# Kernel optimization log

Hardware: AMD Instinct MI355X
Metric: run time of the kernel (lower is better)

Reference implementation:

```python
import jax, jax.numpy as jnp
import numpy as np

EPS_NORM = 1e-12   # torch F.normalize eps
EPS_BN = 1e-5      # BatchNorm1d eps
NEG_SLOPE = 0.01   # LeakyReLU default


def _l2_normalize(x, axis):
    # torch F.normalize: x / max(||x||, eps)
    n = jnp.sqrt(jnp.sum(x * x, axis=axis, keepdims=True))
    return x / jnp.maximum(n, EPS_NORM)


def setup_inputs() -> dict:
    key = jax.random.key(0)
    k1, k2, k3, k4, k5, k6, k7 = jax.random.split(key, 7)
    B, C, N, M, OUT = 8, 128, 4096, 4096, 128
    return {
        "input": jax.random.normal(k1, (B, C, N), dtype=jnp.float32),
        "target_g": jax.random.normal(k2, (B, C, M), dtype=jnp.float32),
        "weight": jax.random.normal(k3, (C, OUT), dtype=jnp.float32) * (1.0 / np.sqrt(OUT)),
        "gamma": jax.random.normal(k4, (OUT,), dtype=jnp.float32),
        "beta": jax.random.normal(k5, (OUT,), dtype=jnp.float32),
        "running_mean": jax.random.normal(k6, (OUT,), dtype=jnp.float32),
        "running_var": jax.random.uniform(k7, (OUT,), dtype=jnp.float32, minval=0.5, maxval=1.5),
    }


def reference(input, target_g, weight, gamma, beta, running_mean, running_var):
    # input: [B, C, N], target_g: [B, C, M]
    # cosine-similarity adjacency: [B, M, N]
    tg = _l2_normalize(target_g, axis=1)
    inp_n = _l2_normalize(input, axis=1)
    adj = jnp.einsum('bcm,bcn->bmn', tg, inp_n)
    adj = jax.nn.softmax(adj, axis=-1)
    # aggregate: [B, M, C]
    agg = jnp.einsum('bmn,bcn->bmc', adj, input)
    # project: [B, M, OUT] -> permute to [B, OUT, M]
    out = jnp.einsum('bmc,co->bom', agg, weight)
    # LeakyReLU then BatchNorm1d (eval mode, running stats)
    out = jnp.where(out >= 0, out, NEG_SLOPE * out)
    inv = jax.lax.rsqrt(running_var + EPS_BN)
    out = (out - running_mean[None, :, None]) * (inv * gamma)[None, :, None] + beta[None, :, None]
    return out
```

## Files before the change

### kernel.cpp

```cpp
#include <hip/hip_runtime.h>
#include <hip/hip_bf16.h>

#define BATCH 8
#define CDIM 128
#define NDIM 4096

typedef __bf16 bf16x8 __attribute__((ext_vector_type(8)));
typedef float f32x4 __attribute__((ext_vector_type(4)));
typedef float f32x16 __attribute__((ext_vector_type(16)));
typedef unsigned u32x4 __attribute__((ext_vector_type(4)));

#define QT_OFF 0u
#define KT_OFF 8388608u
#define VB_OFF 16777216u
#define WT_OFF 25165824u
#define SC_OFF (WT_OFF + 32768u)
#define BI_OFF (SC_OFF + 512u)

__device__ __forceinline__ f32x4 mfma16(bf16x8 a, bf16x8 b, f32x4 c) {
    return __builtin_amdgcn_mfma_f32_16x16x32_bf16(a, b, c, 0, 0, 0);
}
__device__ __forceinline__ f32x16 mfma32(bf16x8 a, bf16x8 b, f32x16 c) {
    return __builtin_amdgcn_mfma_f32_32x32x16_bf16(a, b, c, 0, 0, 0);
}

__device__ __forceinline__ unsigned pack2bf(float a, float b) {
    unsigned short ul = __builtin_bit_cast(unsigned short, (__bf16)a);
    unsigned short uh = __builtin_bit_cast(unsigned short, (__bf16)b);
    return (unsigned)ul | ((unsigned)uh << 16);
}

__device__ __forceinline__ void glds16(const void* g, void* l) {
    __builtin_amdgcn_global_load_lds((__attribute__((address_space(1))) void*)(void*)g,
                                     (__attribute__((address_space(3))) void*)l, 16, 0, 0);
}

__global__ __launch_bounds__(256) void prep_nt(const float* __restrict__ input,
                                               const float* __restrict__ tg,
                                               const float* __restrict__ wgt,
                                               const float* __restrict__ gamma,
                                               const float* __restrict__ beta,
                                               const float* __restrict__ mean,
                                               const float* __restrict__ var,
                                               void* __restrict__ ws) {
    __shared__ float Tt[64][129];
    __shared__ float psum[4][64];
    __shared__ float rn[64];
    const int n0 = blockIdx.x * 64;
    const int b  = blockIdx.y;
    const int tid = threadIdx.x;
    const float* src = (blockIdx.z == 0 ? input : tg) + (size_t)b * CDIM * NDIM;

    #pragma unroll
    for (int i = 0; i < 8; ++i) {
        int f = tid + i * 256;
        int c = f >> 4, j4 = f & 15;
        float4 v = *(const float4*)(src + (size_t)c * NDIM + n0 + j4 * 4);
        Tt[j4 * 4 + 0][c] = v.x;
        Tt[j4 * 4 + 1][c] = v.y;
        Tt[j4 * 4 + 2][c] = v.z;
        Tt[j4 * 4 + 3][c] = v.w;
    }
    __syncthreads();
    {
        int j = tid & 63, part = tid >> 6;
        float ss = 0.f;
        #pragma unroll 8
        for (int c = part * 32; c < part * 32 + 32; ++c) { float x = Tt[j][c]; ss += x * x; }
        psum[part][j] = ss;
    }
    __syncthreads();
    if (tid < 64) {
        float s = psum[0][tid] + psum[1][tid] + psum[2][tid] + psum[3][tid];
        rn[tid] = 1.0f / fmaxf(sqrtf(s), 1e-12f);
    }
    __syncthreads();

    __hip_bfloat16* dstT = (__hip_bfloat16*)((char*)ws + (blockIdx.z == 0 ? KT_OFF : QT_OFF))
                           + ((size_t)b * NDIM + n0) * CDIM;
    #pragma unroll
    for (int i = 0; i < 8; ++i) {
        int f = tid + i * 256;
        int j = f >> 5, c4 = f & 31;
        float r = rn[j];
        float4 v = *(const float4*)&Tt[j][c4 * 4];
        uint2 pk; pk.x = pack2bf(v.x * r, v.y * r); pk.y = pack2bf(v.z * r, v.w * r);
        *(uint2*)((unsigned short*)dstT + (size_t)j * CDIM + c4 * 4) = pk;
    }
    if (blockIdx.z == 0) {
        __hip_bfloat16* vb = (__hip_bfloat16*)((char*)ws + VB_OFF) + (size_t)b * CDIM * NDIM + n0;
        #pragma unroll
        for (int i = 0; i < 8; ++i) {
            int f = tid + i * 256;
            int c = f >> 4, j4 = f & 15;
            float x0 = Tt[j4 * 4 + 0][c], x1 = Tt[j4 * 4 + 1][c];
            float x2 = Tt[j4 * 4 + 2][c], x3 = Tt[j4 * 4 + 3][c];
            uint2 pv; pv.x = pack2bf(x0, x1); pv.y = pack2bf(x2, x3);
            *(uint2*)((unsigned short*)vb + (size_t)c * NDIM + j4 * 4) = pv;
        }
    } else if (blockIdx.x == 0 && b == 0) {
        __hip_bfloat16* wT = (__hip_bfloat16*)((char*)ws + WT_OFF);
        float* sc = (float*)((char*)ws + SC_OFF);
        float* bi = (float*)((char*)ws + BI_OFF);
        #pragma unroll
        for (int i = 0; i < 64; ++i) {
            int f = tid + i * 256;
            int c = f >> 7, o = f & 127;
            wT[o * 128 + c] = __hip_bfloat16(wgt[c * 128 + o]);
        }
        if (tid < 128) {
            float inv = rsqrtf(var[tid] + 1e-5f);
            float s = inv * gamma[tid];
            sc[tid] = s;
            bi[tid] = beta[tid] - mean[tid] * s;
        }
    }
}

__global__ __launch_bounds__(512, 2) void flash5(const void* __restrict__ ws_,
                                                 float* __restrict__ out) {
    extern __shared__ char smem[];
    const char* ws = (const char*)ws_;
    const __hip_bfloat16* Qt = (const __hip_bfloat16*)(ws + QT_OFF);
    const __hip_bfloat16* Kt = (const __hip_bfloat16*)(ws + KT_OFF);
    const __hip_bfloat16* Vb = (const __hip_bfloat16*)(ws + VB_OFF);
    const __hip_bfloat16* wT = (const __hip_bfloat16*)(ws + WT_OFF);
    const float* scale = (const float*)(ws + SC_OFF);
    const float* bias  = (const float*)(ws + BI_OFF);

    const int bx = blockIdx.x;
    const int b  = bx & 7;
    const int m0 = (bx >> 3) * 128;
    const int tid = threadIdx.x;
    const int w = tid >> 6, lane = tid & 63;
    const int hf = lane >> 5;
    const int l31 = lane & 31;
    const int nt = w & 1;
    const int mt = w >> 1;

    const char* kgb = (const char*)(Kt + (size_t)b * NDIM * CDIM);
    const char* vgb = (const char*)(Vb + (size_t)b * CDIM * NDIM);

    bf16x8 qb[8];
    {
        const char* qrow = (const char*)Qt + ((size_t)b * NDIM + m0 + mt * 32 + l31) * 256 + hf * 16;
        #pragma unroll
        for (int s = 0; s < 8; ++s) qb[s] = *(const bf16x8*)(qrow + s * 32);
    }

    unsigned kOff[8];
    {
        int nn = nt * 32 + l31;
        #pragma unroll
        for (int s = 0; s < 8; ++s)
            kOff[s] = nn * 256 + (((2 * s + hf) ^ (nn & 15)) * 16);
    }
    unsigned vOff[2][4];
    #pragma unroll
    for (int t = 0; t < 2; ++t)
        #pragma unroll
        for (int ca = 0; ca < 4; ++ca) {
            int c = ca * 32 + l31;
            vOff[t][ca] = 16384 + c * 128 + (((nt * 4 + t * 2 + hf) ^ (c & 7)) * 16);
        }

    const char* kSrc[2]; const char* vSrc[2];
    unsigned kDst[2], vDst[2];
    #pragma unroll
    for (int i = 0; i < 2; ++i) {
        int slot = i * 512 + tid;
        int n = slot >> 4, j = slot & 15;
        kSrc[i] = kgb + n * 256 + ((j ^ (n & 15)) * 16);
        kDst[i] = i * 8192 + w * 1024;
        int c = slot >> 3, j8 = slot & 7;
        vSrc[i] = vgb + (size_t)c * 8192 + ((j8 ^ (c & 7)) * 16);
        vDst[i] = 16384 + i * 8192 + w * 1024;
    }

    f32x16 oacc[4];
    #pragma unroll
    for (int ca = 0; ca < 4; ++ca)
        #pragma unroll
        for (int i = 0; i < 16; ++i) oacc[ca][i] = 0.f;
    float lacc = 0.f;

    #pragma unroll
    for (int i = 0; i < 2; ++i) { glds16(kSrc[i], smem + kDst[i]); kSrc[i] += 16384; }
    #pragma unroll
    for (int i = 0; i < 2; ++i) { glds16(vSrc[i], smem + vDst[i]); vSrc[i] += 128; }

    auto body = [&](const unsigned bo, const bool do_pref) {
        asm volatile("s_waitcnt vmcnt(0) lgkmcnt(0)\ns_barrier" ::: "memory");
        if (do_pref) {
            const unsigned obo = bo ^ 32768u;
            #pragma unroll
            for (int i = 0; i < 2; ++i) { glds16(kSrc[i], smem + (obo + kDst[i])); kSrc[i] += 16384; }
            #pragma unroll
            for (int i = 0; i < 2; ++i) { glds16(vSrc[i], smem + (obo + vDst[i])); vSrc[i] += 128; }
        }

        f32x16 st;
        #pragma unroll
        for (int i = 0; i < 16; ++i) st[i] = 0.f;
        #pragma unroll
        for (int s = 0; s < 8; ++s) {
            bf16x8 kf = *(const bf16x8*)(smem + bo + kOff[s]);
            st = mfma32(kf, qb[s], st);
        }

        unsigned d[8];
        float lsum = 0.f;
        #pragma unroll
        for (int rq = 0; rq < 4; ++rq) {
            float e0 = __expf(st[rq * 4 + 0] - 1.0f);
            float e1 = __expf(st[rq * 4 + 1] - 1.0f);
            float e2 = __expf(st[rq * 4 + 2] - 1.0f);
            float e3 = __expf(st[rq * 4 + 3] - 1.0f);
            lsum += (e0 + e1) + (e2 + e3);
            d[rq * 2 + 0] = pack2bf(e0, e1);
            d[rq * 2 + 1] = pack2bf(e2, e3);
        }
        lacc += lsum;
        unsigned o[8];
        #pragma unroll
        for (int j = 0; j < 8; ++j) o[j] = (unsigned)__shfl_xor((int)d[j], 32, 64);
        bf16x8 pf[2];
        #pragma unroll
        for (int t = 0; t < 2; ++t) {
            u32x4 tv;
            tv.x = hf ? o[4 * t + 2] : d[4 * t + 0];
            tv.y = hf ? o[4 * t + 3] : d[4 * t + 1];
            tv.z = hf ? d[4 * t + 2] : o[4 * t + 0];
            tv.w = hf ? d[4 * t + 3] : o[4 * t + 1];
            pf[t] = __builtin_bit_cast(bf16x8, tv);
        }

        #pragma unroll
        for (int t = 0; t < 2; ++t) {
            #pragma unroll
            for (int ca = 0; ca < 4; ++ca) {
                bf16x8 vf = *(const bf16x8*)(smem + bo + vOff[t][ca]);
                oacc[ca] = mfma32(vf, pf[t], oacc[ca]);
            }
        }
    };

    for (int ii = 0; ii < 32; ++ii) {
        body(0u, true);
        body(32768u, ii != 31);
    }

    float lw = lacc + __shfl_xor(lacc, 32, 64);
    __syncthreads();
    float* lLds = (float*)(smem + 65536);
    if (lane < 32) lLds[w * 32 + lane] = lw;
    if (w & 1) {
        float4* dst = (float4*)smem + (w >> 1) * 1024 + lane;
        #pragma unroll
        for (int ca = 0; ca < 4; ++ca)
            #pragma unroll
            for (int rq = 0; rq < 4; ++rq) {
                float4 t = { oacc[ca][rq * 4 + 0], oacc[ca][rq * 4 + 1],
                             oacc[ca][rq * 4 + 2], oacc[ca][rq * 4 + 3] };
                dst[(ca * 4 + rq) * 64] = t;
            }
    }
    __syncthreads();
    char* sAgg = smem + 67584;
    if (!(w & 1)) {
        float linv = 1.0f / (lLds[w * 32 + l31] + lLds[(w + 1) * 32 + l31]);
        const float4* srcp = (const float4*)smem + (w >> 1) * 1024 + lane;
        int m = (w >> 1) * 32 + l31;
        char* aggRow = sAgg + m * 256;
        const int mx = (m & 7) << 1;
        #pragma unroll
        for (int ca = 0; ca < 4; ++ca)
            #pragma unroll
            for (int rq = 0; rq < 4; ++rq) {
                float4 ov = srcp[(ca * 4 + rq) * 64];
                float v0 = (oacc[ca][rq * 4 + 0] + ov.x) * linv;
                float v1 = (oacc[ca][rq * 4 + 1] + ov.y) * linv;
                float v2 = (oacc[ca][rq * 4 + 2] + ov.z) * linv;
                float v3 = (oacc[ca][rq * 4 + 3] + ov.w) * linv;
                int cq = ca * 8 + rq * 2 + hf;
                uint2 pk; pk.x = pack2bf(v0, v1); pk.y = pack2bf(v2, v3);
                *(uint2*)(aggRow + ((cq ^ mx) * 8)) = pk;
            }
    }
    __syncthreads();

    const int li = lane & 15, q = lane >> 4;
    const int pm = w * 16 + li;
    f32x4 racc[8];
    #pragma unroll
    for (int ob = 0; ob < 8; ++ob) { racc[ob][0]=0.f; racc[ob][1]=0.f; racc[ob][2]=0.f; racc[ob][3]=0.f; }
    #pragma unroll
    for (int ks = 0; ks < 4; ++ks) {
        int slot8 = ((ks * 4 + q) * 2) ^ ((li & 7) << 1);
        bf16x8 af = *(const bf16x8*)(sAgg + pm * 256 + slot8 * 8);
        #pragma unroll
        for (int ob = 0; ob < 8; ++ob) {
            bf16x8 wf = *(const bf16x8*)((const char*)wT + (ob * 16 + li) * 256 + ks * 64 + q * 16);
            racc[ob] = mfma16(af, wf, racc[ob]);
        }
    }

    float* sRes = (float*)smem;
    #pragma unroll
    for (int ob = 0; ob < 8; ++ob) {
        int oo = ob * 16 + li;
        float sc = scale[oo], bi = bias[oo];
        #pragma unroll
        for (int r = 0; r < 4; ++r) {
            float v = racc[ob][r];
            v = (v >= 0.0f) ? v : 0.01f * v;
            v = v * sc + bi;
            sRes[oo * 132 + w * 16 + q * 4 + r] = v;
        }
    }
    __syncthreads();

    float* outb = out + (size_t)b * CDIM * NDIM + m0;
    #pragma unroll
    for (int i = 0; i < 8; ++i) {
        int f = tid + i * 512;
        int o = f >> 5, mq = f & 31;
        *(float4*)(outb + (size_t)o * NDIM + mq * 4) = *(const float4*)(sRes + o * 132 + mq * 4);
    }
}

extern "C" void kernel_launch(void* const* d_in, const int* in_sizes, int n_in,
                              void* d_out, int out_size, void* d_ws, size_t ws_size,
                              hipStream_t stream) {
    const float* input  = (const float*)d_in[0];
    const float* tg     = (const float*)d_in[1];
    const float* weight = (const float*)d_in[2];
    const float* gamma  = (const float*)d_in[3];
    const float* beta   = (const float*)d_in[4];
    const float* rmean  = (const float*)d_in[5];
    const float* rvar   = (const float*)d_in[6];
    float* out = (float*)d_out;

    (void)in_sizes; (void)n_in; (void)out_size; (void)ws_size;

    hipFuncSetAttribute(reinterpret_cast<const void*>(flash5),
                        hipFuncAttributeMaxDynamicSharedMemorySize, 100352);

    dim3 gprep(NDIM / 64, BATCH, 2);
    prep_nt<<<gprep, 256, 0, stream>>>(input, tg, weight, gamma, beta, rmean, rvar, d_ws);
    flash5<<<dim3(256), 512, 100352, stream>>>(d_ws, out);
}
```

Baseline: 187.5 us.

## Halve flash block to 64 rows, use exp2 with prescaled Q, permlane swap

The flash kernel moves to 256-thread blocks covering 64 query rows, doubling the grid to 512 blocks, with the V tile layout and swizzle rebuilt to match. The log2(e) factor is folded into the normalized target during prep so softmax can use raw v_exp_f32. The fixed -1 shift is dropped, which is safe because cosine scores are bounded and the shift cancels in normalization. The cross-half shuffle is replaced by v_permlane32_swap, and s_setprio is wrapped around the MFMA phases. This aims to raise occupancy and parallelism and cut exp and shuffle overhead, at the cost of re-reading K/V per smaller tile and uncertain correctness of the new tail layouts.

```diff
diff --git a/kernel.cpp b/kernel.cpp
--- a/kernel.cpp
+++ b/kernel.cpp
@@ -33,6 +33,16 @@
 __device__ __forceinline__ void glds16(const void* g, void* l) {
     __builtin_amdgcn_global_load_lds((__attribute__((address_space(1))) void*)(void*)g,
                                      (__attribute__((address_space(3))) void*)l, 16, 0, 0);
+}
+
+__device__ __forceinline__ void pls32(unsigned& a, unsigned& b) {
+    asm("v_permlane32_swap_b32 %0, %1" : "+v"(a), "+v"(b));
+}
+
+__device__ __forceinline__ float vexp2(float x) {
+    float r;
+    asm("v_exp_f32 %0, %1" : "=v"(r) : "v"(x));
+    return r;
 }
 
 __global__ __launch_bounds__(256) void prep_nt(const float* __restrict__ input,
@@ -50,6 +60,7 @@
     const int b  = blockIdx.y;
     const int tid = threadIdx.x;
     const float* src = (blockIdx.z == 0 ? input : tg) + (size_t)b * CDIM * NDIM;
+    const float zscale = (blockIdx.z == 0) ? 1.0f : 1.4426950408889634f;
 
     #pragma unroll
     for (int i = 0; i < 8; ++i) {
@@ -82,7 +93,7 @@
     for (int i = 0; i < 8; ++i) {
         int f = tid + i * 256;
         int j = f >> 5, c4 = f & 31;
-        float r = rn[j];
+        float r = rn[j] * zscale;
         float4 v = *(const float4*)&Tt[j][c4 * 4];
         uint2 pk; pk.x = pack2bf(v.x * r, v.y * r); pk.y = pack2bf(v.z * r, v.w * r);
         *(uint2*)((unsigned short*)dstT + (size_t)j * CDIM + c4 * 4) = pk;
@@ -117,7 +128,7 @@
     }
 }
 
-__global__ __launch_bounds__(512, 2) void flash5(const void* __restrict__ ws_,
+__global__ __launch_bounds__(256, 2) void flash7(const void* __restrict__ ws_,
                                                  float* __restrict__ out) {
     extern __shared__ char smem[];
     const char* ws = (const char*)ws_;
@@ -130,7 +141,7 @@
 
     const int bx = blockIdx.x;
     const int b  = bx & 7;
-    const int m0 = (bx >> 3) * 128;
+    const int m0 = (bx >> 3) * 64;
     const int tid = threadIdx.x;
     const int w = tid >> 6, lane = tid & 63;
     const int hf = lane >> 5;
@@ -161,21 +172,23 @@
         #pragma unroll
         for (int ca = 0; ca < 4; ++ca) {
             int c = ca * 32 + l31;
-            vOff[t][ca] = 16384 + c * 128 + (((nt * 4 + t * 2 + hf) ^ (c & 7)) * 16);
-        }
-
-    const char* kSrc[2]; const char* vSrc[2];
-    unsigned kDst[2], vDst[2];
-    #pragma unroll
-    for (int i = 0; i < 2; ++i) {
-        int slot = i * 512 + tid;
-        int n = slot >> 4, j = slot & 15;
-        kSrc[i] = kgb + n * 256 + ((j ^ (n & 15)) * 16);
-        kDst[i] = i * 8192 + w * 1024;
-        int c = slot >> 3, j8 = slot & 7;
-        vSrc[i] = vgb + (size_t)c * 8192 + ((j8 ^ (c & 7)) * 16);
-        vDst[i] = 16384 + i * 8192 + w * 1024;
-    }
+            int rr = c >> 1;
+            int sl = (((c & 1) << 3) | (nt * 4 + t * 2 + hf)) ^ (rr & 15);
+            vOff[t][ca] = 16384 + rr * 256 + sl * 16;
+        }
+
+    unsigned kLane[4], vLane[4];
+    #pragma unroll
+    for (int i = 0; i < 4; ++i) {
+        int slot = i * 256 + tid;
+        int r = slot >> 4, j = slot & 15;
+        kLane[i] = r * 256 + ((j ^ (r & 15)) * 16);
+        int u = j ^ (r & 15);
+        int c = r * 2 + (u >> 3), ch = u & 7;
+        vLane[i] = c * 8192 + ch * 16;
+    }
+    const unsigned kDstB = w * 1024;
+    const unsigned vDstB = 16384 + w * 1024;
 
     f32x16 oacc[4];
     #pragma unroll
@@ -185,64 +198,72 @@
     float lacc = 0.f;
 
     #pragma unroll
-    for (int i = 0; i < 2; ++i) { glds16(kSrc[i], smem + kDst[i]); kSrc[i] += 16384; }
-    #pragma unroll
-    for (int i = 0; i < 2; ++i) { glds16(vSrc[i], smem + vDst[i]); vSrc[i] += 128; }
+    for (int i = 0; i < 4; ++i) glds16(kgb + kLane[i], smem + kDstB + i * 4096);
+    #pragma unroll
+    for (int i = 0; i < 4; ++i) glds16(vgb + vLane[i], smem + vDstB + i * 4096);
+    unsigned kOffG = 16384;
+    unsigned vOffG = 128;
+
+    auto softmax_pf = [&](const f32x16& s, bf16x8* pf) {
+        unsigned d[8];
+        float lsum = 0.f;
+        #pragma unroll
+        for (int rq = 0; rq < 4; ++rq) {
+            float e0 = vexp2(s[rq * 4 + 0]);
+            float e1 = vexp2(s[rq * 4 + 1]);
+            float e2 = vexp2(s[rq * 4 + 2]);
+            float e3 = vexp2(s[rq * 4 + 3]);
+            lsum += (e0 + e1) + (e2 + e3);
+            d[rq * 2 + 0] = pack2bf(e0, e1);
+            d[rq * 2 + 1] = pack2bf(e2, e3);
+        }
+        lacc += lsum;
+        #pragma unroll
+        for (int t = 0; t < 2; ++t) {
+            pls32(d[4 * t + 0], d[4 * t + 2]);
+            pls32(d[4 * t + 1], d[4 * t + 3]);
+            u32x4 tv;
+            tv.x = d[4 * t + 0]; tv.y = d[4 * t + 1];
+            tv.z = d[4 * t + 2]; tv.w = d[4 * t + 3];
+            pf[t] = __builtin_bit_cast(bf16x8, tv);
+        }
+    };
 
     auto body = [&](const unsigned bo, const bool do_pref) {
         asm volatile("s_waitcnt vmcnt(0) lgkmcnt(0)\ns_barrier" ::: "memory");
         if (do_pref) {
             const unsigned obo = bo ^ 32768u;
             #pragma unroll
-            for (int i = 0; i < 2; ++i) { glds16(kSrc[i], smem + (obo + kDst[i])); kSrc[i] += 16384; }
-            #pragma unroll
-            for (int i = 0; i < 2; ++i) { glds16(vSrc[i], smem + (obo + vDst[i])); vSrc[i] += 128; }
+            for (int i = 0; i < 4; ++i) glds16(kgb + kOffG + kLane[i], smem + (obo + kDstB + i * 4096));
+            #pragma unroll
+            for (int i = 0; i < 4; ++i) glds16(vgb + vOffG + vLane[i], smem + (obo + vDstB + i * 4096));
+            kOffG += 16384;
+            vOffG += 128;
         }
 
         f32x16 st;
         #pragma unroll
         for (int i = 0; i < 16; ++i) st[i] = 0.f;
+        __builtin_amdgcn_s_setprio(1);
         #pragma unroll
         for (int s = 0; s < 8; ++s) {
             bf16x8 kf = *(const bf16x8*)(smem + bo + kOff[s]);
             st = mfma32(kf, qb[s], st);
         }
-
-        unsigned d[8];
-        float lsum = 0.f;
-        #pragma unroll
-        for (int rq = 0; rq < 4; ++rq) {
-            float e0 = __expf(st[rq * 4 + 0] - 1.0f);
-            float e1 = __expf(st[rq * 4 + 1] - 1.0f);
-            float e2 = __expf(st[rq * 4 + 2] - 1.0f);
-            float e3 = __expf(st[rq * 4 + 3] - 1.0f);
-            lsum += (e0 + e1) + (e2 + e3);
-            d[rq * 2 + 0] = pack2bf(e0, e1);
-            d[rq * 2 + 1] = pack2bf(e2, e3);
-        }
-        lacc += lsum;
-        unsigned o[8];
-        #pragma unroll
-        for (int j = 0; j < 8; ++j) o[j] = (unsigned)__shfl_xor((int)d[j], 32, 64);
+        __builtin_amdgcn_s_setprio(0);
+
         bf16x8 pf[2];
-        #pragma unroll
-        for (int t = 0; t < 2; ++t) {
-            u32x4 tv;
-            tv.x = hf ? o[4 * t + 2] : d[4 * t + 0];
-            tv.y = hf ? o[4 * t + 3] : d[4 * t + 1];
-            tv.z = hf ? d[4 * t + 2] : o[4 * t + 0];
-            tv.w = hf ? d[4 * t + 3] : o[4 * t + 1];
-            pf[t] = __builtin_bit_cast(bf16x8, tv);
-        }
-
-        #pragma unroll
-        for (int t = 0; t < 2; ++t) {
+        softmax_pf(st, pf);
+
+        __builtin_amdgcn_s_setprio(1);
+        #pragma unroll
+        for (int t = 0; t < 2; ++t)
             #pragma unroll
             for (int ca = 0; ca < 4; ++ca) {
                 bf16x8 vf = *(const bf16x8*)(smem + bo + vOff[t][ca]);
                 oacc[ca] = mfma32(vf, pf[t], oacc[ca]);
             }
-        }
+        __builtin_amdgcn_s_setprio(0);
     };
 
     for (int ii = 0; ii < 32; ++ii) {
@@ -252,7 +273,7 @@
 
     float lw = lacc + __shfl_xor(lacc, 32, 64);
     __syncthreads();
-    float* lLds = (float*)(smem + 65536);
+    float* lLds = (float*)(smem + 32768);
     if (lane < 32) lLds[w * 32 + lane] = lw;
     if (w & 1) {
         float4* dst = (float4*)smem + (w >> 1) * 1024 + lane;
@@ -266,7 +287,7 @@
             }
     }
     __syncthreads();
-    char* sAgg = smem + 67584;
+    char* sAgg = smem + 36864;
     if (!(w & 1)) {
         float linv = 1.0f / (lLds[w * 32 + l31] + lLds[(w + 1) * 32 + l31]);
         const float4* srcp = (const float4*)smem + (w >> 1) * 1024 + lane;
@@ -315,7 +336,7 @@
             float v = racc[ob][r];
             v = (v >= 0.0f) ? v : 0.01f * v;
             v = v * sc + bi;
-            sRes[oo * 132 + w * 16 + q * 4 + r] = v;
+            sRes[oo * 72 + w * 16 + q * 4 + r] = v;
         }
     }
     __syncthreads();
@@ -323,9 +344,9 @@
     float* outb = out + (size_t)b * CDIM * NDIM + m0;
     #pragma unroll
     for (int i = 0; i < 8; ++i) {
-        int f = tid + i * 512;
-        int o = f >> 5, mq = f & 31;
-        *(float4*)(outb + (size_t)o * NDIM + mq * 4) = *(const float4*)(sRes + o * 132 + mq * 4);
+        int f = tid + i * 256;
+        int o = f >> 4, mq = f & 15;
+        *(float4*)(outb + (size_t)o * NDIM + mq * 4) = *(const float4*)(sRes + o * 72 + mq * 4);
     }
 }
 
@@ -343,10 +364,10 @@
 
     (void)in_sizes; (void)n_in; (void)out_size; (void)ws_size;
 
-    hipFuncSetAttribute(reinterpret_cast<const void*>(flash5),
-                        hipFuncAttributeMaxDynamicSharedMemorySize, 100352);
+    hipFuncSetAttribute(reinterpret_cast<const void*>(flash7),
+                        hipFuncAttributeMaxDynamicSharedMemorySize, 65536);
 
     dim3 gprep(NDIM / 64, BATCH, 2);
     prep_nt<<<gprep, 256, 0, stream>>>(input, tg, weight, gamma, beta, rmean, rvar, d_ws);
-    flash5<<<dim3(256), 512, 100352, stream>>>(d_ws, out);
-}
+    flash7<<<dim3(512), 256, 65536, stream>>>(d_ws, out);
+}
```

Result: no change. 189.2 us (+0.9%).

## Load K/V fragments directly from global memory and swap halves with permlane32

Applied to the files above, without the earlier changes.

Removes the double-buffered LDS staging of K and V tiles (global_load_lds plus barriers) and has each wave load its MFMA operand fragments straight from global memory. It also replaces the shfl_xor-based exchange of softmax probabilities between half-waves with v_permlane32_swap. This drops the per-iteration barriers and LDS traffic, at the cost of redundant global/L2 reads across waves and no explicit prefetch to hide load latency.

```diff
diff --git a/kernel.cpp b/kernel.cpp
--- a/kernel.cpp
+++ b/kernel.cpp
@@ -30,9 +30,8 @@
     return (unsigned)ul | ((unsigned)uh << 16);
 }
 
-__device__ __forceinline__ void glds16(const void* g, void* l) {
-    __builtin_amdgcn_global_load_lds((__attribute__((address_space(1))) void*)(void*)g,
-                                     (__attribute__((address_space(3))) void*)l, 16, 0, 0);
+__device__ __forceinline__ void pls32(unsigned& a, unsigned& b) {
+    asm("v_permlane32_swap_b32 %0, %1" : "+v"(a), "+v"(b));
 }
 
 __global__ __launch_bounds__(256) void prep_nt(const float* __restrict__ input,
@@ -117,8 +116,8 @@
     }
 }
 
-__global__ __launch_bounds__(512, 2) void flash5(const void* __restrict__ ws_,
-                                                 float* __restrict__ out) {
+__global__ __launch_bounds__(512, 2) void flash12(const void* __restrict__ ws_,
+                                                  float* __restrict__ out) {
     extern __shared__ char smem[];
     const char* ws = (const char*)ws_;
     const __hip_bfloat16* Qt = (const __hip_bfloat16*)(ws + QT_OFF);
@@ -148,34 +147,11 @@
         for (int s = 0; s < 8; ++s) qb[s] = *(const bf16x8*)(qrow + s * 32);
     }
 
-    unsigned kOff[8];
-    {
-        int nn = nt * 32 + l31;
-        #pragma unroll
-        for (int s = 0; s < 8; ++s)
-            kOff[s] = nn * 256 + (((2 * s + hf) ^ (nn & 15)) * 16);
-    }
-    unsigned vOff[2][4];
-    #pragma unroll
-    for (int t = 0; t < 2; ++t)
-        #pragma unroll
-        for (int ca = 0; ca < 4; ++ca) {
-            int c = ca * 32 + l31;
-            vOff[t][ca] = 16384 + c * 128 + (((nt * 4 + t * 2 + hf) ^ (c & 7)) * 16);
-        }
-
-    const char* kSrc[2]; const char* vSrc[2];
-    unsigned kDst[2], vDst[2];
-    #pragma unroll
-    for (int i = 0; i < 2; ++i) {
-        int slot = i * 512 + tid;
-        int n = slot >> 4, j = slot & 15;
-        kSrc[i] = kgb + n * 256 + ((j ^ (n & 15)) * 16);
-        kDst[i] = i * 8192 + w * 1024;
-        int c = slot >> 3, j8 = slot & 7;
-        vSrc[i] = vgb + (size_t)c * 8192 + ((j8 ^ (c & 7)) * 16);
-        vDst[i] = 16384 + i * 8192 + w * 1024;
-    }
+    const char* kPtr = kgb + (size_t)(nt * 32 + l31) * 256 + hf * 16;
+    const char* vPtr[4];
+    #pragma unroll
+    for (int ca = 0; ca < 4; ++ca)
+        vPtr[ca] = vgb + (size_t)(ca * 32 + l31) * 8192 + nt * 64 + hf * 16;
 
     f32x16 oacc[4];
     #pragma unroll
@@ -184,70 +160,55 @@
         for (int i = 0; i < 16; ++i) oacc[ca][i] = 0.f;
     float lacc = 0.f;
 
-    #pragma unroll
-    for (int i = 0; i < 2; ++i) { glds16(kSrc[i], smem + kDst[i]); kSrc[i] += 16384; }
-    #pragma unroll
-    for (int i = 0; i < 2; ++i) { glds16(vSrc[i], smem + vDst[i]); vSrc[i] += 128; }
-
-    auto body = [&](const unsigned bo, const bool do_pref) {
-        asm volatile("s_waitcnt vmcnt(0) lgkmcnt(0)\ns_barrier" ::: "memory");
-        if (do_pref) {
-            const unsigned obo = bo ^ 32768u;
-            #pragma unroll
-            for (int i = 0; i < 2; ++i) { glds16(kSrc[i], smem + (obo + kDst[i])); kSrc[i] += 16384; }
-            #pragma unroll
-            for (int i = 0; i < 2; ++i) { glds16(vSrc[i], smem + (obo + vDst[i])); vSrc[i] += 128; }
-        }
-
-        f32x16 st;
-        #pragma unroll
-        for (int i = 0; i < 16; ++i) st[i] = 0.f;
-        #pragma unroll
-        for (int s = 0; s < 8; ++s) {
-            bf16x8 kf = *(const bf16x8*)(smem + bo + kOff[s]);
-            st = mfma32(kf, qb[s], st);
-        }
-
+    auto softmax_pf = [&](const f32x16& s, bf16x8* pf) {
         unsigned d[8];
         float lsum = 0.f;
         #pragma unroll
         for (int rq = 0; rq < 4; ++rq) {
-            float e0 = __expf(st[rq * 4 + 0] - 1.0f);
-            float e1 = __expf(st[rq * 4 + 1] - 1.0f);
-            float e2 = __expf(st[rq * 4 + 2] - 1.0f);
-            float e3 = __expf(st[rq * 4 + 3] - 1.0f);
+            float e0 = __expf(s[rq * 4 + 0] - 1.0f);
+            float e1 = __expf(s[rq * 4 + 1] - 1.0f);
+            float e2 = __expf(s[rq * 4 + 2] - 1.0f);
+            float e3 = __expf(s[rq * 4 + 3] - 1.0f);
             lsum += (e0 + e1) + (e2 + e3);
             d[rq * 2 + 0] = pack2bf(e0, e1);
             d[rq * 2 + 1] = pack2bf(e2, e3);
         }
         lacc += lsum;
-        unsigned o[8];
-        #pragma unroll
-        for (int j = 0; j < 8; ++j) o[j] = (unsigned)__shfl_xor((int)d[j], 32, 64);
+        #pragma unroll
+        for (int t = 0; t < 2; ++t) {
+            pls32(d[4 * t + 0], d[4 * t + 2]);
+            pls32(d[4 * t + 1], d[4 * t + 3]);
+            u32x4 tv;
+            tv.x = d[4 * t + 0]; tv.y = d[4 * t + 1];
+            tv.z = d[4 * t + 2]; tv.w = d[4 * t + 3];
+            pf[t] = __builtin_bit_cast(bf16x8, tv);
+        }
+    };
+
+    for (int i = 0; i < 64; ++i) {
+        bf16x8 kf[8];
+        #pragma unroll
+        for (int s = 0; s < 8; ++s) kf[s] = *(const bf16x8*)(kPtr + s * 32);
+        f32x16 st;
+        #pragma unroll
+        for (int j = 0; j < 16; ++j) st[j] = 0.f;
+        #pragma unroll
+        for (int s = 0; s < 8; ++s) st = mfma32(kf[s], qb[s], st);
+
         bf16x8 pf[2];
-        #pragma unroll
-        for (int t = 0; t < 2; ++t) {
-            u32x4 tv;
-            tv.x = hf ? o[4 * t + 2] : d[4 * t + 0];
-            tv.y = hf ? o[4 * t + 3] : d[4 * t + 1];
-            tv.z = hf ? d[4 * t + 2] : o[4 * t + 0];
-            tv.w = hf ? d[4 * t + 3] : o[4 * t + 1];
-            pf[t] = __builtin_bit_cast(bf16x8, tv);
-        }
-
-        #pragma unroll
-        for (int t = 0; t < 2; ++t) {
+        softmax_pf(st, pf);
+
+        #pragma unroll
+        for (int t = 0; t < 2; ++t)
             #pragma unroll
             for (int ca = 0; ca < 4; ++ca) {
-                bf16x8 vf = *(const bf16x8*)(smem + bo + vOff[t][ca]);
+                bf16x8 vf = *(const bf16x8*)(vPtr[ca] + t * 32);
                 oacc[ca] = mfma32(vf, pf[t], oacc[ca]);
             }
-        }
-    };
-
-    for (int ii = 0; ii < 32; ++ii) {
-        body(0u, true);
-        body(32768u, ii != 31);
+
+        kPtr += 16384;
+        #pragma unroll
+        for (int ca = 0; ca < 4; ++ca) vPtr[ca] += 128;
     }
 
     float lw = lacc + __shfl_xor(lacc, 32, 64);
@@ -343,10 +304,10 @@
 
     (void)in_sizes; (void)n_in; (void)out_size; (void)ws_size;
 
-    hipFuncSetAttribute(reinterpret_cast<const void*>(flash5),
+    hipFuncSetAttribute(reinterpret_cast<const void*>(flash12),
                         hipFuncAttributeMaxDynamicSharedMemorySize, 100352);
 
     dim3 gprep(NDIM / 64, BATCH, 2);
     prep_nt<<<gprep, 256, 0, stream>>>(input, tg, weight, gamma, beta, rmean, rvar, d_ws);
-    flash5<<<dim3(256), 512, 100352, stream>>>(d_ws, out);
-}
+    flash12<<<dim3(256), 512, 100352, stream>>>(d_ws, out);
+}
```

After: 385.3 us. 106% more time.
